# Kernel tuning notes

Hardware: AMD Instinct MI355X
Metric: run time of the kernel (lower is better)

Reference implementation:

```python
import jax, jax.numpy as jnp
import numpy as np

B, S, H, F, E, K = 2, 2048, 1024, 4096, 8, 2


def setup_inputs() -> dict:
    key = jax.random.key(0)
    ks = jax.random.split(key, 5)
    scale = 0.02
    return {
        "hidden_states": jax.random.normal(ks[0], (B, S, H), jnp.float32),
        "gate_w": jax.random.normal(ks[1], (H, E), jnp.float32) * scale,  # nn.Linear(H,E,bias=False)
        "w1": jax.random.normal(ks[2], (E, H, F), jnp.float32) * scale,   # per-expert fc1
        "b1": jnp.zeros((E, F), jnp.float32),
        "w2": jax.random.normal(ks[3], (E, F, H), jnp.float32) * scale,   # per-expert fc2
        "b2": jnp.zeros((E, H), jnp.float32),
    }


def reference(hidden_states, gate_w, w1, b1, w2, b2):
    b, s, h = hidden_states.shape
    x = hidden_states.reshape(b * s, h)  # [T, H]
    T = x.shape[0]
    n_experts = gate_w.shape[1]

    # --- Top-K gating ---
    router_logits = x @ gate_w                      # [T, E]
    router_probs = jax.nn.softmax(router_logits, axis=-1)
    topk_probs, topk_idx = jax.lax.top_k(router_probs, K)  # [T, K]
    topk_probs = topk_probs / topk_probs.sum(axis=-1, keepdims=True)
    aux_loss = n_experts * jnp.sum(router_probs.mean(axis=0) ** 2)

    # --- Combine weights: scatter normalized top-k probs into dense [T, E] ---
    combine_w = jnp.zeros((T, n_experts), x.dtype).at[
        jnp.arange(T)[:, None], topk_idx
    ].add(topk_probs)

    # --- Expert MLPs (dense per-expert batched GEMM; zero combine weight drops unrouted) ---
    hidden = jax.nn.relu(jnp.einsum('th,ehf->etf', x, w1) + b1[:, None, :])  # [E, T, F]
    expert_out = jnp.einsum('etf,efh->eth', hidden, w2) + b2[:, None, :]     # [E, T, H]

    out = jnp.einsum('te,eth->th', combine_w, expert_out)  # weighted combine
    return out.reshape(b, s, h), aux_loss
```

## Files before the change

kernel.cpp:

```cpp
#include <hip/hip_runtime.h>
#include <hip/hip_bf16.h>
#include <cstdint>

#define AS1 __attribute__((address_space(1)))
#define AS3 __attribute__((address_space(3)))

typedef __attribute__((ext_vector_type(8))) short short8x;
typedef __attribute__((ext_vector_type(4))) float f32x4;

static constexpr int T    = 4096;
static constexpr int HD   = 1024;
static constexpr int FD   = 4096;
static constexpr int NE   = 8;
static constexpr int P    = T * 2;
static constexpr int PPAD = P + 128;
static constexpr int MAXTILES = P / 128 + NE;
static constexpr int RTB  = 16;
static constexpr int RNB  = T / RTB;

struct TileDesc { int e; int start; int rows; int pad; };

__device__ __forceinline__ uint16_t f2bf(float f) {
  uint32_t u = __builtin_bit_cast(uint32_t, f);
  u += 0x7FFFu + ((u >> 16) & 1u);
  return (uint16_t)(u >> 16);
}
__device__ __forceinline__ float bf2f(uint16_t b) {
  uint32_t u = ((uint32_t)b) << 16;
  return __builtin_bit_cast(float, u);
}

__device__ __forceinline__ void gload_lds16(const void* g, void* l) {
  __builtin_amdgcn_global_load_lds((const AS1 uint32_t*)g, (AS3 uint32_t*)l, 16, 0, 0);
}

__global__ __launch_bounds__(256) void cvt_x_kernel(const float* __restrict__ x,
                                                    uint16_t* __restrict__ xb) {
  size_t i = ((size_t)blockIdx.x * 256 + threadIdx.x) * 4;
  float4 v = *(const float4*)&x[i];
  ushort4 o;
  o.x = f2bf(v.x); o.y = f2bf(v.y); o.z = f2bf(v.z); o.w = f2bf(v.w);
  *(ushort4*)&xb[i] = o;
}

__global__ __launch_bounds__(256) void transpose_cvt_kernel(
    const float* __restrict__ in, uint16_t* __restrict__ out, int R, int C) {
  __shared__ float tile[32][33];
  int z = blockIdx.z;
  const float* inp = in + (size_t)z * R * C;
  uint16_t* outp = out + (size_t)z * R * C;
  int tx = threadIdx.x, ty = threadIdx.y;
  int r0 = blockIdx.y * 32, c0 = blockIdx.x * 32;
#pragma unroll
  for (int j = 0; j < 4; ++j)
    tile[ty + 8 * j][tx] = inp[(size_t)(r0 + ty + 8 * j) * C + (c0 + tx)];
  __syncthreads();
#pragma unroll
  for (int j = 0; j < 4; ++j)
    outp[(size_t)(c0 + ty + 8 * j) * R + (r0 + tx)] = f2bf(tile[tx][ty + 8 * j]);
}

__global__ __launch_bounds__(256) void router_kernel(
    const float* __restrict__ x, const float* __restrict__ gate_w,
    int* __restrict__ topk_idx, float* __restrict__ topk_w,
    float* __restrict__ part_sums, int* __restrict__ part_counts) {
  __shared__ float g[NE * HD];
  __shared__ float ls[NE];
  __shared__ int   lc[NE];
  int tid = threadIdx.x;
  for (int i = tid; i < NE * HD; i += 256)
    g[(i & 7) * HD + (i >> 3)] = gate_w[i];
  if (tid < NE) { ls[tid] = 0.f; lc[tid] = 0; }
  __syncthreads();
  int wave = tid >> 6, lane = tid & 63;
  float psum[NE];
#pragma unroll
  for (int e = 0; e < NE; ++e) psum[e] = 0.f;

  for (int tt = 0; tt < RTB / 4; ++tt) {
    int t = blockIdx.x * RTB + wave * (RTB / 4) + tt;
    const float* xr = x + (size_t)t * HD;
    float acc[NE];
#pragma unroll
    for (int e = 0; e < NE; ++e) acc[e] = 0.f;
    for (int i = 0; i < HD / 64; ++i) {
      float xv = xr[lane + i * 64];
#pragma unroll
      for (int e = 0; e < NE; ++e) acc[e] += xv * g[e * HD + lane + i * 64];
    }
#pragma unroll
    for (int off = 32; off > 0; off >>= 1)
#pragma unroll
      for (int e = 0; e < NE; ++e) acc[e] += __shfl_down(acc[e], off);
    if (lane == 0) {
      float m = acc[0];
#pragma unroll
      for (int e = 1; e < NE; ++e) m = fmaxf(m, acc[e]);
      float p[NE], s = 0.f;
#pragma unroll
      for (int e = 0; e < NE; ++e) { p[e] = expf(acc[e] - m); s += p[e]; }
      float inv = 1.f / s;
#pragma unroll
      for (int e = 0; e < NE; ++e) { p[e] *= inv; psum[e] += p[e]; }
      int i0 = 0;
#pragma unroll
      for (int e = 1; e < NE; ++e) if (p[e] > p[i0]) i0 = e;
      int i1 = (i0 == 0) ? 1 : 0;
#pragma unroll
      for (int e = 0; e < NE; ++e) if (e != i0 && e != i1 && p[e] > p[i1]) i1 = e;
      float wsum = p[i0] + p[i1];
      topk_idx[t * 2] = i0; topk_idx[t * 2 + 1] = i1;
      topk_w[t * 2] = p[i0] / wsum; topk_w[t * 2 + 1] = p[i1] / wsum;
      atomicAdd(&lc[i0], 1); atomicAdd(&lc[i1], 1);
    }
  }
  if (lane == 0)
#pragma unroll
    for (int e = 0; e < NE; ++e) atomicAdd(&ls[e], psum[e]);
  __syncthreads();
  if (tid < NE) {
    part_sums[blockIdx.x * NE + tid]   = ls[tid];
    part_counts[blockIdx.x * NE + tid] = lc[tid];
  }
}

__global__ __launch_bounds__(64) void finalize_kernel(
    const int* __restrict__ part_counts, const float* __restrict__ part_sums,
    int* __restrict__ offsets, TileDesc* __restrict__ desc,
    int* __restrict__ ntiles, float* __restrict__ aux_out) {
  __shared__ int   csh[NE];
  __shared__ float ssh[NE];
  int tid = threadIdx.x;
  if (tid < NE) {
    int c = 0; float s = 0.f;
    for (int b = 0; b < RNB; ++b) {
      c += part_counts[b * NE + tid];
      s += part_sums[b * NE + tid];
    }
    csh[tid] = c; ssh[tid] = s;
  }
  __syncthreads();
  if (tid == 0) {
    int off = 0, nt = 0;
    for (int e = 0; e < NE; ++e) {
      offsets[e] = off;
      int c = csh[e];
      for (int i = 0; i < c; i += 128) {
        int rows = c - i; if (rows > 128) rows = 128;
        desc[nt].e = e; desc[nt].start = off + i; desc[nt].rows = rows; desc[nt].pad = 0;
        nt++;
      }
      off += c;
    }
    *ntiles = nt;
    float aux = 0.f;
    for (int e = 0; e < NE; ++e) {
      float mean = ssh[e] / (float)T;
      aux += mean * mean;
    }
    *aux_out = (float)NE * aux;
  }
}

__global__ __launch_bounds__(256) void scatter_kernel(
    const int* __restrict__ topk_idx, const int* __restrict__ offsets,
    int* __restrict__ fill, int* __restrict__ pair_tok, int* __restrict__ tok_pos) {
  int t = blockIdx.x * 256 + threadIdx.x;
  int lane = threadIdx.x & 63;
  unsigned long long below = (lane == 63) ? ~0ull >> 1
                                          : ((1ull << (lane + 1)) - 1) >> 1;
#pragma unroll
  for (int k = 0; k < 2; ++k) {
    int e = topk_idx[t * 2 + k];
    int pos = 0;
    for (int ex = 0; ex < NE; ++ex) {
      unsigned long long m = __ballot(e == ex);
      if (e == ex) {
        int leader = __ffsll((long long)m) - 1;
        int cnt = __popcll(m);
        int base = 0;
        if (lane == leader) base = atomicAdd(&fill[ex], cnt);
        base = __shfl(base, leader);
        pos = base + __popcll(m & below);
      }
    }
    int pp = offsets[e] + pos;
    pair_tok[pp] = t;
    tok_pos[t * 2 + k] = pp;
  }
}

template <int KD, int ND, int EPI>
__global__ __launch_bounds__(256) void moe_gemm(
    const uint16_t* __restrict__ Abase, const int* __restrict__ pair_tok,
    const uint16_t* __restrict__ Bw, const float* __restrict__ bias,
    uint16_t* __restrict__ Cout, const TileDesc* __restrict__ desc,
    const int* __restrict__ ntiles) {
  int mt = blockIdx.y;
  if (mt >= *ntiles) return;
  TileDesc d = desc[mt];
  int nb = blockIdx.x;

  __shared__ uint16_t As[128 * 32];
  __shared__ uint16_t Bs[128 * 32];
  __shared__ int rowA[128];

  int tid = threadIdx.x, lane = tid & 63, wave = tid >> 6;
  int wm = wave >> 1, wn = wave & 1;

  int idx0 = (wave * 2 + 0) * 64 + lane;
  int idx1 = (wave * 2 + 1) * 64 + lane;
  int ar0 = idx0 >> 2, kc0 = idx0 & 3;
  int ar1 = idx1 >> 2, kc1 = idx1 & 3;

  int ra0, ra1;
  if constexpr (EPI == 0) {
    if (tid < 128) rowA[tid] = (tid < d.rows) ? pair_tok[d.start + tid] : 0;
    __syncthreads();
    ra0 = rowA[ar0]; ra1 = rowA[ar1];
  } else {
    ra0 = d.start + ar0; ra1 = d.start + ar1;
  }

  const uint16_t* Bbase = Bw + ((size_t)d.e * ND + (size_t)nb * 128) * KD;

  f32x4 acc[4][4];
#pragma unroll
  for (int i = 0; i < 4; ++i)
#pragma unroll
    for (int j = 0; j < 4; ++j) acc[i][j] = (f32x4){0.f, 0.f, 0.f, 0.f};

  for (int kt = 0; kt < KD / 32; ++kt) {
    if (kt) __syncthreads();
    int kb = kt * 32;
    gload_lds16(Abase + (size_t)ra0 * KD + kb + kc0 * 8, &As[(wave * 2 + 0) * 512]);
    gload_lds16(Abase + (size_t)ra1 * KD + kb + kc1 * 8, &As[(wave * 2 + 1) * 512]);
    gload_lds16(Bbase + (size_t)ar0 * KD + kb + kc0 * 8, &Bs[(wave * 2 + 0) * 512]);
    gload_lds16(Bbase + (size_t)ar1 * KD + kb + kc1 * 8, &Bs[(wave * 2 + 1) * 512]);
    __syncthreads();

    short8x af[4], bfr[4];
#pragma unroll
    for (int i = 0; i < 4; ++i)
      af[i] = *(const short8x*)&As[(wm * 64 + i * 16 + (lane & 15)) * 32 + (lane >> 4) * 8];
#pragma unroll
    for (int j = 0; j < 4; ++j)
      bfr[j] = *(const short8x*)&Bs[(wn * 64 + j * 16 + (lane & 15)) * 32 + (lane >> 4) * 8];
#pragma unroll
    for (int i = 0; i < 4; ++i)
#pragma unroll
      for (int j = 0; j < 4; ++j)
        acc[i][j] = __builtin_amdgcn_mfma_f32_16x16x32_bf16(af[i], bfr[j], acc[i][j], 0, 0, 0);
  }

  int rq = (lane >> 4) * 4;
  int cl = lane & 15;
#pragma unroll
  for (int i = 0; i < 4; ++i) {
    int rb = wm * 64 + i * 16 + rq;
#pragma unroll
    for (int j = 0; j < 4; ++j) {
      int col = nb * 128 + wn * 64 + j * 16 + cl;
      float bv = bias[d.e * ND + col];
#pragma unroll
      for (int q = 0; q < 4; ++q) {
        int r = rb + q;
        if (r < d.rows) {
          float v = acc[i][j][q] + bv;
          if (EPI == 0) v = fmaxf(v, 0.f);
          Cout[(size_t)(d.start + r) * ND + col] = f2bf(v);
        }
      }
    }
  }
}

__global__ __launch_bounds__(256) void combine_kernel(
    const uint16_t* __restrict__ po, const int* __restrict__ tok_pos,
    const float* __restrict__ topk_w, float* __restrict__ out) {
  int t = blockIdx.x;
  int c = threadIdx.x * 4;
  int p0 = tok_pos[t * 2], p1 = tok_pos[t * 2 + 1];
  float w0 = topk_w[t * 2], w1 = topk_w[t * 2 + 1];
  ushort4 a = *(const ushort4*)&po[(size_t)p0 * HD + c];
  ushort4 b = *(const ushort4*)&po[(size_t)p1 * HD + c];
  float4 o;
  o.x = w0 * bf2f(a.x) + w1 * bf2f(b.x);
  o.y = w0 * bf2f(a.y) + w1 * bf2f(b.y);
  o.z = w0 * bf2f(a.z) + w1 * bf2f(b.z);
  o.w = w0 * bf2f(a.w) + w1 * bf2f(b.w);
  *(float4*)&out[(size_t)t * HD + c] = o;
}

extern "C" void kernel_launch(void* const* d_in, const int* in_sizes, int n_in,
                              void* d_out, int out_size, void* d_ws, size_t ws_size,
                              hipStream_t stream) {
  const float* x      = (const float*)d_in[0];
  const float* gate_w = (const float*)d_in[1];
  const float* w1     = (const float*)d_in[2];
  const float* b1     = (const float*)d_in[3];
  const float* w2     = (const float*)d_in[4];
  const float* b2     = (const float*)d_in[5];
  float* out = (float*)d_out;
  (void)in_sizes; (void)n_in; (void)out_size; (void)ws_size;

  char* w = (char*)d_ws;
  size_t off = 0;
  auto alloc = [&](size_t bytes) -> void* {
    void* p = w + off;
    off = (off + bytes + 255) & ~(size_t)255;
    return p;
  };
  int*      meta     = (int*)alloc(256);
  int*      fill     = meta;
  int*      offsets  = (int*)alloc(256);
  int*      ntiles   = offsets + 8;
  TileDesc* desc     = (TileDesc*)alloc(sizeof(TileDesc) * 128);
  int*      topk_idx = (int*)alloc(sizeof(int) * P);
  float*    topk_w   = (float*)alloc(sizeof(float) * P);
  int*      tok_pos  = (int*)alloc(sizeof(int) * P);
  int*      pair_tok = (int*)alloc(sizeof(int) * PPAD);
  float*    psums    = (float*)alloc(sizeof(float) * RNB * NE);
  int*      pcounts  = (int*)alloc(sizeof(int) * RNB * NE);
  uint16_t* xb       = (uint16_t*)alloc((size_t)T * HD * 2);
  uint16_t* w1t      = (uint16_t*)alloc((size_t)NE * FD * HD * 2);
  uint16_t* w2t      = (uint16_t*)alloc((size_t)NE * HD * FD * 2);
  uint16_t* hidden   = (uint16_t*)alloc((size_t)PPAD * FD * 2);
  uint16_t* pout     = (uint16_t*)alloc((size_t)PPAD * HD * 2);

  hipMemsetAsync(meta, 0, 256, stream);
  cvt_x_kernel<<<(T * HD) / 1024, 256, 0, stream>>>(x, xb);
  transpose_cvt_kernel<<<dim3(FD / 32, HD / 32, NE), dim3(32, 8), 0, stream>>>(w1, w1t, HD, FD);
  transpose_cvt_kernel<<<dim3(HD / 32, FD / 32, NE), dim3(32, 8), 0, stream>>>(w2, w2t, FD, HD);
  router_kernel<<<RNB, 256, 0, stream>>>(x, gate_w, topk_idx, topk_w, psums, pcounts);
  finalize_kernel<<<1, 64, 0, stream>>>(pcounts, psums, offsets, desc, ntiles,
                                        out + (size_t)T * HD);
  scatter_kernel<<<T / 256, 256, 0, stream>>>(topk_idx, offsets, fill, pair_tok, tok_pos);
  moe_gemm<HD, FD, 0><<<dim3(FD / 128, MAXTILES), 256, 0, stream>>>(
      xb, pair_tok, w1t, b1, hidden, desc, ntiles);
  moe_gemm<FD, HD, 1><<<dim3(HD / 128, MAXTILES), 256, 0, stream>>>(
      hidden, pair_tok, w2t, b2, pout, desc, ntiles);
  combine_kernel<<<T, 256, 0, stream>>>(pout, tok_pos, topk_w, out);
}
```

Before: 390.2 us.

## Double-buffer MoE GEMM LDS, swizzle block order, and widen transpose tiles

The MoE GEMM now double-buffers its A/B LDS tiles, so the next K-slice's global-to-LDS loads are issued before the MFMAs on the current slice, with one barrier per iteration. The grid is flattened and remapped so blocks are spread across XCDs and grouped by M-tile for L2 reuse of weight tiles. The weight transpose-convert kernel moves to 64x64 tiles with float4 reads and ushort4 writes. Together these aim to hide load latency, improve cache locality, and cut memory transactions, at the cost of twice the LDS per block (which may lower occupancy) and a possible race from issuing async loads into the other buffer with only one sync per step.

```diff
diff --git a/kernel.cpp b/kernel.cpp
--- a/kernel.cpp
+++ b/kernel.cpp
@@ -45,19 +45,33 @@
 
 __global__ __launch_bounds__(256) void transpose_cvt_kernel(
     const float* __restrict__ in, uint16_t* __restrict__ out, int R, int C) {
-  __shared__ float tile[32][33];
+  __shared__ float tile[64][65];
   int z = blockIdx.z;
   const float* inp = in + (size_t)z * R * C;
   uint16_t* outp = out + (size_t)z * R * C;
-  int tx = threadIdx.x, ty = threadIdx.y;
-  int r0 = blockIdx.y * 32, c0 = blockIdx.x * 32;
-#pragma unroll
-  for (int j = 0; j < 4; ++j)
-    tile[ty + 8 * j][tx] = inp[(size_t)(r0 + ty + 8 * j) * C + (c0 + tx)];
-  __syncthreads();
-#pragma unroll
-  for (int j = 0; j < 4; ++j)
-    outp[(size_t)(c0 + ty + 8 * j) * R + (r0 + tx)] = f2bf(tile[tx][ty + 8 * j]);
+  int r0 = blockIdx.y * 64, c0 = blockIdx.x * 64;
+  int tid = threadIdx.x;
+  int lr = tid >> 4;
+  int lc4 = (tid & 15) * 4;
+#pragma unroll
+  for (int p = 0; p < 4; ++p) {
+    float4 v = *(const float4*)&inp[(size_t)(r0 + lr + p * 16) * C + c0 + lc4];
+    tile[lr + p * 16][lc4 + 0] = v.x;
+    tile[lr + p * 16][lc4 + 1] = v.y;
+    tile[lr + p * 16][lc4 + 2] = v.z;
+    tile[lr + p * 16][lc4 + 3] = v.w;
+  }
+  __syncthreads();
+#pragma unroll
+  for (int p = 0; p < 4; ++p) {
+    int c = lr + p * 16;
+    ushort4 o;
+    o.x = f2bf(tile[lc4 + 0][c]);
+    o.y = f2bf(tile[lc4 + 1][c]);
+    o.z = f2bf(tile[lc4 + 2][c]);
+    o.w = f2bf(tile[lc4 + 3][c]);
+    *(ushort4*)&outp[(size_t)(c0 + c) * R + r0 + lc4] = o;
+  }
 }
 
 __global__ __launch_bounds__(256) void router_kernel(
@@ -196,13 +210,22 @@
     const uint16_t* __restrict__ Bw, const float* __restrict__ bias,
     uint16_t* __restrict__ Cout, const TileDesc* __restrict__ desc,
     const int* __restrict__ ntiles) {
-  int mt = blockIdx.y;
+  constexpr int NB = ND / 128;
+  constexpr int TOTAL = NB * MAXTILES;
+  constexpr int SM = 8;
+
+  int orig = blockIdx.x;
+  int work = (orig & 7) * (TOTAL / 8) + (orig >> 3);
+  int srow = work / (SM * NB);
+  int rem  = work % (SM * NB);
+  int nb   = rem / SM;
+  int mt   = srow * SM + (rem & (SM - 1));
+
   if (mt >= *ntiles) return;
   TileDesc d = desc[mt];
-  int nb = blockIdx.x;
-
-  __shared__ uint16_t As[128 * 32];
-  __shared__ uint16_t Bs[128 * 32];
+
+  __shared__ uint16_t As[2][128 * 32];
+  __shared__ uint16_t Bs[2][128 * 32];
   __shared__ int rowA[128];
 
   int tid = threadIdx.x, lane = tid & 63, wave = tid >> 6;
@@ -223,6 +246,18 @@
   }
 
   const uint16_t* Bbase = Bw + ((size_t)d.e * ND + (size_t)nb * 128) * KD;
+  const uint16_t* Arow0 = Abase + (size_t)ra0 * KD + kc0 * 8;
+  const uint16_t* Arow1 = Abase + (size_t)ra1 * KD + kc1 * 8;
+  const uint16_t* Brow0 = Bbase + (size_t)ar0 * KD + kc0 * 8;
+  const uint16_t* Brow1 = Bbase + (size_t)ar1 * KD + kc1 * 8;
+
+  auto stage = [&](int buf, int kt) {
+    int kb = kt * 32;
+    gload_lds16(Arow0 + kb, &As[buf][(wave * 2 + 0) * 512]);
+    gload_lds16(Arow1 + kb, &As[buf][(wave * 2 + 1) * 512]);
+    gload_lds16(Brow0 + kb, &Bs[buf][(wave * 2 + 0) * 512]);
+    gload_lds16(Brow1 + kb, &Bs[buf][(wave * 2 + 1) * 512]);
+  };
 
   f32x4 acc[4][4];
 #pragma unroll
@@ -230,27 +265,28 @@
 #pragma unroll
     for (int j = 0; j < 4; ++j) acc[i][j] = (f32x4){0.f, 0.f, 0.f, 0.f};
 
-  for (int kt = 0; kt < KD / 32; ++kt) {
-    if (kt) __syncthreads();
-    int kb = kt * 32;
-    gload_lds16(Abase + (size_t)ra0 * KD + kb + kc0 * 8, &As[(wave * 2 + 0) * 512]);
-    gload_lds16(Abase + (size_t)ra1 * KD + kb + kc1 * 8, &As[(wave * 2 + 1) * 512]);
-    gload_lds16(Bbase + (size_t)ar0 * KD + kb + kc0 * 8, &Bs[(wave * 2 + 0) * 512]);
-    gload_lds16(Bbase + (size_t)ar1 * KD + kb + kc1 * 8, &Bs[(wave * 2 + 1) * 512]);
-    __syncthreads();
+  constexpr int NT = KD / 32;
+  stage(0, 0);
+  __syncthreads();
+
+  for (int kt = 0; kt < NT; ++kt) {
+    int cur = kt & 1;
+    if (kt + 1 < NT) stage(cur ^ 1, kt + 1);
 
     short8x af[4], bfr[4];
 #pragma unroll
     for (int i = 0; i < 4; ++i)
-      af[i] = *(const short8x*)&As[(wm * 64 + i * 16 + (lane & 15)) * 32 + (lane >> 4) * 8];
+      af[i] = *(const short8x*)&As[cur][(wm * 64 + i * 16 + (lane & 15)) * 32 + (lane >> 4) * 8];
 #pragma unroll
     for (int j = 0; j < 4; ++j)
-      bfr[j] = *(const short8x*)&Bs[(wn * 64 + j * 16 + (lane & 15)) * 32 + (lane >> 4) * 8];
+      bfr[j] = *(const short8x*)&Bs[cur][(wn * 64 + j * 16 + (lane & 15)) * 32 + (lane >> 4) * 8];
 #pragma unroll
     for (int i = 0; i < 4; ++i)
 #pragma unroll
       for (int j = 0; j < 4; ++j)
         acc[i][j] = __builtin_amdgcn_mfma_f32_16x16x32_bf16(af[i], bfr[j], acc[i][j], 0, 0, 0);
+
+    __syncthreads();
   }
 
   int rq = (lane >> 4) * 4;
@@ -330,15 +366,15 @@
 
   hipMemsetAsync(meta, 0, 256, stream);
   cvt_x_kernel<<<(T * HD) / 1024, 256, 0, stream>>>(x, xb);
-  transpose_cvt_kernel<<<dim3(FD / 32, HD / 32, NE), dim3(32, 8), 0, stream>>>(w1, w1t, HD, FD);
-  transpose_cvt_kernel<<<dim3(HD / 32, FD / 32, NE), dim3(32, 8), 0, stream>>>(w2, w2t, FD, HD);
+  transpose_cvt_kernel<<<dim3(FD / 64, HD / 64, NE), 256, 0, stream>>>(w1, w1t, HD, FD);
+  transpose_cvt_kernel<<<dim3(HD / 64, FD / 64, NE), 256, 0, stream>>>(w2, w2t, FD, HD);
   router_kernel<<<RNB, 256, 0, stream>>>(x, gate_w, topk_idx, topk_w, psums, pcounts);
   finalize_kernel<<<1, 64, 0, stream>>>(pcounts, psums, offsets, desc, ntiles,
                                         out + (size_t)T * HD);
   scatter_kernel<<<T / 256, 256, 0, stream>>>(topk_idx, offsets, fill, pair_tok, tok_pos);
-  moe_gemm<HD, FD, 0><<<dim3(FD / 128, MAXTILES), 256, 0, stream>>>(
+  moe_gemm<HD, FD, 0><<<(FD / 128) * MAXTILES, 256, 0, stream>>>(
       xb, pair_tok, w1t, b1, hidden, desc, ntiles);
-  moe_gemm<FD, HD, 1><<<dim3(HD / 128, MAXTILES), 256, 0, stream>>>(
+  moe_gemm<FD, HD, 1><<<(HD / 128) * MAXTILES, 256, 0, stream>>>(
       hidden, pair_tok, w2t, b2, pout, desc, ntiles);
   combine_kernel<<<T, 256, 0, stream>>>(pout, tok_pos, topk_w, out);
 }
```

Result: slower. 422.2 us (+8.2%).
